# Optimization experiments

Measured on AMD Instinct MI355X. Metric: run time of the kernel, lower is better.

Reference implementation:

```python
import jax, jax.numpy as jnp
import numpy as np

HIDDEN = 384
NDIM = 3
N_POINTS = 100000
N_SUPER = 2048
MAX_DEG = 32
RADIUS = 0.045
INPUT_DIM = 3


def _sincos_embed(coords):
    # ContinuousSincosEmbed: dim=384, ndim=3 -> 128 channels per spatial dim (64 sin + 64 cos)
    eff = HIDDEN // NDIM  # 128
    omega = jnp.arange(0, eff, 2, dtype=jnp.float32) / eff
    freq = 1.0 / (10000.0 ** omega)  # [eff//2]
    out = coords[..., None] * freq  # [..., ndim, eff//2]
    emb = jnp.concatenate([jnp.sin(out), jnp.cos(out)], axis=-1)  # [..., ndim, eff]
    return emb.reshape(coords.shape[:-1] + (HIDDEN,))


def _radius_neighbors(pos, sn_idx):
    # numpy preprocessing equivalent of torch_geometric.nn.pool.radius with
    # max_num_neighbors=MAX_DEG; fixed-size padded [S, K] output + validity mask.
    nbr = np.zeros((N_SUPER, MAX_DEG), np.int32)
    mask = np.zeros((N_SUPER, MAX_DEG), bool)
    pos2 = (pos ** 2).sum(-1)
    r2 = RADIUS * RADIUS
    chunk = 128
    for i0 in range(0, N_SUPER, chunk):
        sp = pos[sn_idx[i0:i0 + chunk]]
        d2 = (sp ** 2).sum(-1)[:, None] + pos2[None, :] - 2.0 * (sp @ pos.T)
        within = d2 <= r2
        for j in range(sp.shape[0]):
            idx = np.nonzero(within[j])[0][:MAX_DEG]
            nbr[i0 + j, :len(idx)] = idx
            mask[i0 + j, :len(idx)] = True
    return nbr, mask


def setup_inputs() -> dict:
    rng = np.random.default_rng(0)
    pos = rng.random((N_POINTS, NDIM)).astype(np.float32)
    sn_idx = np.sort(rng.choice(N_POINTS, N_SUPER, replace=False)).astype(np.int32)
    nbr, mask = _radius_neighbors(pos, sn_idx)
    key = jax.random.key(0)
    ks = jax.random.split(key, 6)
    s = 0.02  # truncnormal002 init scale
    return {
        "input_pos": jnp.asarray(pos),
        "input_feat": jax.random.normal(ks[0], (N_POINTS, INPUT_DIM), jnp.float32),
        "supernode_idx": jnp.asarray(sn_idx),
        "neighbor_idx": jnp.asarray(nbr),
        "neighbor_mask": jnp.asarray(mask),
        "W_in": jax.random.normal(ks[1], (INPUT_DIM, HIDDEN), jnp.float32) * s,
        "b_in": jnp.zeros((HIDDEN,), jnp.float32),
        "W1": jax.random.normal(ks[2], (2 * HIDDEN, HIDDEN), jnp.float32) * s,
        "b1": jnp.zeros((HIDDEN,), jnp.float32),
        "W2": jax.random.normal(ks[3], (HIDDEN, HIDDEN), jnp.float32) * s,
        "b2": jnp.zeros((HIDDEN,), jnp.float32),
        "W_proj": jax.random.normal(ks[4], (2 * HIDDEN, HIDDEN), jnp.float32) * s,
        "b_proj": jnp.zeros((HIDDEN,), jnp.float32),
    }


def reference(input_pos, input_feat, supernode_idx, neighbor_idx, neighbor_mask,
              W_in, b_in, W1, b1, W2, b2, W_proj, b_proj):
    # point embeddings: continuous sincos pos embed + input feature projection
    x = _sincos_embed(input_pos) + input_feat @ W_in + b_in          # [N, D]
    sn = x[supernode_idx]                                            # [S, D] supernode pos embed
    src = x[neighbor_idx]                                            # [S, K, D] gathered neighbors
    dst = jnp.broadcast_to(sn[:, None, :], src.shape)                # [S, K, D]
    h = jnp.concatenate([src, dst], axis=-1)                         # [S, K, 2D]
    # message MLP (Linear -> GELU(exact) -> Linear), as nn.GELU default
    h = jax.nn.gelu(h @ W1 + b1, approximate=False) @ W2 + b2        # [S, K, D]
    # masked mean == segment_csr(..., reduce='mean') over variable-degree edges
    m = neighbor_mask[..., None].astype(h.dtype)
    agg = (h * m).sum(axis=1) / jnp.maximum(m.sum(axis=1), 1.0)      # [S, D]
    # readd_supernode_pos: concat supernode pos embed, project 2D -> D
    out = jnp.concatenate([agg, sn], axis=-1) @ W_proj + b_proj      # [S, D]
    return out[None]                                                 # [1, S, D] (batch_size=1)
```

## Files before the change

### kernel.cpp

```cpp
#include <hip/hip_runtime.h>
#include <hip/hip_bf16.h>
#include <cstdint>

#define HIDDEN 384
#define NSUPER 2048
#define MAXDEG 32
#define FRAGS (12*24*64)
#define WBLK  (FRAGS*8)

typedef __attribute__((ext_vector_type(8))) short bf16x8;
typedef __attribute__((ext_vector_type(4))) float f32x4;

__device__ inline unsigned short f2bf(float f) {
    __hip_bfloat16 h = __float2bfloat16(f);
    return *reinterpret_cast<unsigned short*>(&h);
}
__device__ inline float b2f(unsigned short s) {
    return __uint_as_float(((unsigned int)s) << 16);
}
__device__ inline bf16x8 pack8(const float* v) {
    union { bf16x8 v8; unsigned short u[8]; } u;
    #pragma unroll
    for (int i = 0; i < 8; ++i) u.u[i] = f2bf(v[i]);
    return u.v8;
}
__device__ inline float fast_erf(float x) {
    float ax = fabsf(x);
    float t  = 1.0f / fmaf(0.3275911f, ax, 1.0f);
    float p  = t*(0.254829592f + t*(-0.284496736f + t*(1.421413741f +
               t*(-1.453152027f + t*1.061405429f))));
    float e  = __expf(-ax*ax);
    return copysignf(1.0f - p*e, x);
}
__device__ inline float gelu(float y) {
    return 0.5f * y * (1.0f + fast_erf(y * 0.70710678118654752f));
}

__global__ __launch_bounds__(256)
void prep(const float* __restrict__ W1, const float* __restrict__ W2,
          const float* __restrict__ Wp, const unsigned int* __restrict__ mask,
          const float* __restrict__ pos, const float* __restrict__ feat,
          const int* __restrict__ sn_idx,
          const float* __restrict__ W_in, const float* __restrict__ b_in,
          unsigned short* __restrict__ w1sf, unsigned short* __restrict__ w1df,
          unsigned short* __restrict__ w2f,  unsigned short* __restrict__ wpf,
          unsigned short* __restrict__ snxb, int* __restrict__ flag) {
    const int b = blockIdx.x;
    const int t = threadIdx.x;
    if (b == 360) {
        __shared__ int s;
        if (t == 0) s = 0;
        __syncthreads();
        int bad = 0;
        for (int i = t; i < 16384; i += 256)
            if (mask[i] > 1u) bad = 1;
        if (bad) s = 1;
        __syncthreads();
        if (t == 0) *flag = s;
        return;
    }
    if (b > 360) {
        __shared__ float W4[HIDDEN][4];
        __shared__ float P6[64][7];
        const int eb = b - 361;
        if (t < 64) {
            const int pi = sn_idx[eb*64 + t];
            P6[t][0]=pos[pi*3];  P6[t][1]=pos[pi*3+1];  P6[t][2]=pos[pi*3+2];
            P6[t][3]=feat[pi*3]; P6[t][4]=feat[pi*3+1]; P6[t][5]=feat[pi*3+2];
        }
        for (int d = t; d < HIDDEN; d += 256) {
            W4[d][0]=W_in[d]; W4[d][1]=W_in[HIDDEN+d];
            W4[d][2]=W_in[2*HIDDEN+d]; W4[d][3]=b_in[d];
        }
        __syncthreads();
        const int er = t >> 2, seg = t & 3;
        float frA[8], frB[8];
        #pragma unroll
        for (int i = 0; i < 8; ++i) {
            frA[i] = exp2f(-(float)(seg*8 + i)      * 0.2076205059304601f);
            frB[i] = exp2f(-(float)(32 + seg*8 + i) * 0.2076205059304601f);
        }
        const float f0 = P6[er][3], f1 = P6[er][4], f2 = P6[er][5];
        #pragma unroll
        for (int cc = 0; cc < 3; ++cc) {
            const float pc = P6[er][cc];
            float sL[8], sH[8], cL[8], cH[8];
            #pragma unroll
            for (int i = 0; i < 8; ++i) {
                const float aL = pc*frA[i], aH = pc*frB[i];
                sL[i]=__sinf(aL); sH[i]=__sinf(aH); cL[i]=__cosf(aL); cH[i]=__cosf(aH);
            }
            #pragma unroll
            for (int q = 0; q < 4; ++q) {
                const float* bb = (q==0)?sL:(q==1)?sH:(q==2)?cL:cH;
                const int blk = cc*4 + q;
                float v[8];
                #pragma unroll
                for (int i = 0; i < 8; ++i) {
                    const int dim = blk*32 + seg*8 + i;
                    const float4 wv = *(const float4*)W4[dim];
                    v[i] = fmaf(f0, wv.x, fmaf(f1, wv.y, fmaf(f2, wv.z, bb[i] + wv.w)));
                }
                *(bf16x8*)&snxb[(size_t)(eb*64 + er)*HIDDEN + blk*32 + seg*8] = pack8(v);
            }
        }
        return;
    }
    const int grp = b / 72, sub = b % 72;
    const float* W; unsigned short* out;
    switch (grp) {
        case 0: W = W1;              out = w1sf; break;
        case 1: W = W1 + 384*HIDDEN; out = w1df; break;
        case 2: W = W2;              out = w2f;  break;
        case 3: W = Wp;              out = wpf;  break;
        default:W = Wp + 384*HIDDEN; out = wpf + WBLK; break;
    }
    const int idx = sub * 256 + t;
    const int l   = idx & 63;
    const int frag= idx >> 6;
    const int nt  = frag % 24;
    const int kt  = frag / 24;
    const int col = nt * 16 + (l & 15);
    const int k0  = kt * 32 + (l >> 4) * 8;
    unsigned int pk[4];
    #pragma unroll
    for (int j = 0; j < 4; ++j) {
        unsigned int lo = f2bf(W[(k0 + 2*j)     * HIDDEN + col]);
        unsigned int hi = f2bf(W[(k0 + 2*j + 1) * HIDDEN + col]);
        pk[j] = lo | (hi << 16);
    }
    *reinterpret_cast<uint4*>(&out[(size_t)idx * 8]) =
        *reinterpret_cast<const uint4*>(pk);
}

__global__ __launch_bounds__(256)
void k_dstv(const unsigned short* __restrict__ snxb,
            const unsigned short* __restrict__ w1df,
            const float* __restrict__ b1, float* __restrict__ dstv) {
    const int rg = blockIdx.x >> 2, cq = blockIdx.x & 3;
    const int t = threadIdx.x, w = t>>6, l = t&63, lg = l>>4, l15 = l&15;
    const int wgm = w>>1, wgn = w&1;
    const int r0 = rg*64 + wgm*32;
    const int ntb = cq*6 + wgn*3;
    f32x4 acc[2][3];
    #pragma unroll
    for (int mt=0; mt<2; ++mt)
        #pragma unroll
        for (int nt=0; nt<3; ++nt) acc[mt][nt] = (f32x4){0.f,0.f,0.f,0.f};
    #pragma unroll 2
    for (int kt = 0; kt < 12; ++kt) {
        bf16x8 a[2], bfr[3];
        const unsigned short* bpp = &w1df[((size_t)(kt*24 + ntb)*64 + l)*8];
        #pragma unroll
        for (int nt=0; nt<3; ++nt) bfr[nt] = *(const bf16x8*)(bpp + (size_t)nt*512);
        #pragma unroll
        for (int mt=0; mt<2; ++mt)
            a[mt] = *(const bf16x8*)&snxb[(size_t)(r0 + mt*16 + l15)*HIDDEN + kt*32 + lg*8];
        #pragma unroll
        for (int mt=0; mt<2; ++mt)
            #pragma unroll
            for (int nt=0; nt<3; ++nt)
                acc[mt][nt] = __builtin_amdgcn_mfma_f32_16x16x32_bf16(a[mt], bfr[nt], acc[mt][nt], 0,0,0);
    }
    #pragma unroll
    for (int mt=0; mt<2; ++mt)
        #pragma unroll
        for (int nt=0; nt<3; ++nt) {
            const int col = cq*96 + wgn*48 + nt*16 + l15;
            #pragma unroll
            for (int r=0; r<4; ++r) {
                const int row = r0 + mt*16 + lg*4 + r;
                dstv[(size_t)row*HIDDEN + col] = acc[mt][nt][r] + b1[col];
            }
        }
}

__global__ __launch_bounds__(256, 2)
void k_mlp(const float* __restrict__ pos, const float* __restrict__ feat,
           const int* __restrict__ nbr_idx, const void* __restrict__ mask_raw,
           const int* __restrict__ mask_fmt,
           const float* __restrict__ W_in, const float* __restrict__ b_in,
           const float* __restrict__ dstv,
           const unsigned short* __restrict__ W1f,
           const unsigned short* __restrict__ W2f,
           const float* __restrict__ b2, unsigned short* __restrict__ aggb)
{
    __shared__ unsigned short G[4*12*64*8];
    __shared__ ushort4 WINTB[HIDDEN];
    __shared__ float PF[64][7];
    __shared__ float CNT[2];

    const int t  = threadIdx.x;
    const int bm = blockIdx.x;
    const int l = t & 63, ng = t >> 6, lg = l >> 4, l15 = l & 15;

    float dvreg[2][6];
    #pragma unroll
    for (int sl = 0; sl < 2; ++sl)
        #pragma unroll
        for (int nt = 0; nt < 6; ++nt)
            dvreg[sl][nt] = dstv[(size_t)(bm*2 + sl)*HIDDEN + ng*96 + nt*16 + l15];

    bf16x8 bA[6], bB[6];
    #define LOADB(dst, Wf, kt)                                                  \
        { const unsigned short* bp_ = &Wf[((size_t)((kt)*24 + ng*6)*64 + l)*8]; \
          _Pragma("unroll")                                                     \
          for (int nt_ = 0; nt_ < 6; ++nt_)                                     \
              dst[nt_] = *(const bf16x8*)(bp_ + (size_t)nt_*512); }
    #define AREAD(a_, kt)                                                       \
        { _Pragma("unroll")                                                     \
          for (int mt_ = 0; mt_ < 4; ++mt_)                                     \
              a_[mt_] = *(const bf16x8*)&G[(size_t)(((mt_*12 + (kt))*64) + l)*8]; }
    #define MFMA6(bfr, a_)                                                      \
        { __builtin_amdgcn_s_setprio(1);                                        \
          _Pragma("unroll")                                                     \
          for (int mt_ = 0; mt_ < 4; ++mt_)                                     \
              _Pragma("unroll")                                                 \
              for (int nt_ = 0; nt_ < 6; ++nt_)                                 \
                  acc[mt_][nt_] = __builtin_amdgcn_mfma_f32_16x16x32_bf16(      \
                      a_[mt_], bfr[nt_], acc[mt_][nt_], 0, 0, 0);               \
          __builtin_amdgcn_s_setprio(0); }

    LOADB(bA, W1f, 0);

    if (t < 64) {
        const int e  = bm*64 + t;
        const int pi = nbr_idx[e];
        PF[t][0]=pos[pi*3];  PF[t][1]=pos[pi*3+1];  PF[t][2]=pos[pi*3+2];
        PF[t][3]=feat[pi*3]; PF[t][4]=feat[pi*3+1]; PF[t][5]=feat[pi*3+2];
        const int fmt = *mask_fmt;
        const int mv  = fmt ? (int)((const unsigned char*)mask_raw)[e]
                            : ((const int*)mask_raw)[e];
        PF[t][6] = mv ? 1.0f : 0.0f;
    }
    for (int d = t; d < HIDDEN; d += 256) {
        ushort4 wv;
        wv.x = f2bf(W_in[d]); wv.y = f2bf(W_in[HIDDEN+d]);
        wv.z = f2bf(W_in[2*HIDDEN+d]); wv.w = f2bf(b_in[d]);
        WINTB[d] = wv;
    }
    __syncthreads();
    if (t < 2) {
        float c = 0.f;
        for (int s = 0; s < 32; ++s) c += PF[t*32+s][6];
        CNT[t] = c;
    }

    const int er = t >> 2, seg = t & 3;
    float frA[8], frB[8];
    #pragma unroll
    for (int i = 0; i < 8; ++i) {
        frA[i] = exp2f(-(float)(seg*8 + i)      * 0.2076205059304601f);
        frB[i] = exp2f(-(float)(32 + seg*8 + i) * 0.2076205059304601f);
    }
    const float f0 = PF[er][3], f1 = PF[er][4], f2 = PF[er][5];
    const float pc0 = PF[er][0], pc1 = PF[er][1], pc2 = PF[er][2];
    const int slotbase = (er>>4)*12*64 + seg*16 + (er&15);

    #define EMB(kt_)                                                            \
        { const float pc = ((kt_)>>2)==0 ? pc0 : (((kt_)>>2)==1 ? pc1 : pc2);   \
          float v[8];                                                           \
          _Pragma("unroll")                                                     \
          for (int i = 0; i < 8; ++i) {                                         \
              const float fr = ((kt_)&1) ? frB[i] : frA[i];                     \
              const float aa = pc * fr;                                         \
              const float base = (((kt_)>>1)&1) ? __cosf(aa) : __sinf(aa);      \
              const ushort4 wv = WINTB[(kt_)*32 + seg*8 + i];                   \
              v[i] = fmaf(f0, b2f(wv.x), fmaf(f1, b2f(wv.y),                    \
                     fmaf(f2, b2f(wv.z), base + b2f(wv.w))));                   \
          }                                                                     \
          *(bf16x8*)&G[(size_t)(slotbase + (kt_)*64)*8] = pack8(v); }

    EMB(0);
    __syncthreads();

    f32x4 acc[4][6];
    #pragma unroll
    for (int mt=0; mt<4; ++mt)
        #pragma unroll
        for (int nt=0; nt<6; ++nt) acc[mt][nt] = (f32x4){0.f,0.f,0.f,0.f};

    #pragma unroll
    for (int kt = 0; kt < 12; kt += 2) {
        bf16x8 a[4];
        AREAD(a, kt);
        LOADB(bB, W1f, kt + 1);
        EMB(kt + 1);
        MFMA6(bA, a);
        __syncthreads();
        AREAD(a, kt + 1);
        if (kt + 2 < 12) { LOADB(bA, W1f, kt + 2); EMB(kt + 2); }
        MFMA6(bB, a);
        __syncthreads();
    }

    #pragma unroll
    for (int mt=0; mt<4; ++mt) {
        const int sl = mt >> 1;
        #pragma unroll
        for (int nt=0; nt<6; ++nt) {
            const int col = ng*96 + nt*16 + l15;
            const float dv = dvreg[sl][nt];
            const int base = ((mt*12 + (col>>5))*64 + ((col>>3)&3)*16 + lg*4)*8 + (col&7);
            #pragma unroll
            for (int r=0; r<4; ++r)
                G[base + r*8] = f2bf(gelu(acc[mt][nt][r] + dv));
        }
    }
    __syncthreads();

    #pragma unroll
    for (int mt=0; mt<4; ++mt)
        #pragma unroll
        for (int nt=0; nt<6; ++nt) acc[mt][nt] = (f32x4){0.f,0.f,0.f,0.f};
    LOADB(bA, W2f, 0); LOADB(bB, W2f, 1);
    #pragma unroll
    for (int kt = 0; kt < 12; kt += 2) {
        bf16x8 a[4];
        AREAD(a, kt);
        MFMA6(bA, a);
        if (kt + 2 < 12) LOADB(bA, W2f, kt + 2);
        AREAD(a, kt + 1);
        MFMA6(bB, a);
        if (kt + 3 < 12) LOADB(bB, W2f, kt + 3);
    }

    #pragma unroll
    for (int nt=0; nt<6; ++nt) {
        const int col = ng*96 + nt*16 + l15;
        float s0 = 0.f, s1 = 0.f;
        #pragma unroll
        for (int mt=0; mt<4; ++mt) {
            float p = 0.f;
            #pragma unroll
            for (int r=0; r<4; ++r)
                p += PF[mt*16 + lg*4 + r][6] * acc[mt][nt][r];
            if (mt < 2) s0 += p; else s1 += p;
        }
        s0 += __shfl_xor(s0,16); s0 += __shfl_xor(s0,32);
        s1 += __shfl_xor(s1,16); s1 += __shfl_xor(s1,32);
        if (lg == 0) {
            const float bb = b2[col];
            const int sn0 = bm*2;
            const float c0 = CNT[0], c1 = CNT[1];
            aggb[(size_t)sn0*HIDDEN + col]     = f2bf(s0 / fmaxf(c0,1.f) + bb*(c0>0.f?1.f:0.f));
            aggb[(size_t)(sn0+1)*HIDDEN + col] = f2bf(s1 / fmaxf(c1,1.f) + bb*(c1>0.f?1.f:0.f));
        }
    }
    #undef LOADB
    #undef AREAD
    #undef MFMA6
    #undef EMB
}

__global__ __launch_bounds__(256)
void k_proj(const unsigned short* __restrict__ aggb,
            const unsigned short* __restrict__ snxb,
            const unsigned short* __restrict__ wpf,
            const float* __restrict__ bp, float* __restrict__ out) {
    const int rg = blockIdx.x >> 2, cq = blockIdx.x & 3;
    const int t = threadIdx.x, w = t>>6, l = t&63, lg = l>>4, l15 = l&15;
    const int wgm = w>>1, wgn = w&1;
    const int r0 = rg*64 + wgm*32;
    const int ntb = cq*6 + wgn*3;
    f32x4 acc[2][3];
    #pragma unroll
    for (int mt=0; mt<2; ++mt)
        #pragma unroll
        for (int nt=0; nt<3; ++nt) acc[mt][nt] = (f32x4){0.f,0.f,0.f,0.f};
    #pragma unroll 2
    for (int kt = 0; kt < 24; ++kt) {
        const unsigned short* Ab = (kt < 12) ? aggb : snxb;
        const unsigned short* Wb = (kt < 12) ? wpf  : wpf + WBLK;
        const int ktt = (kt < 12) ? kt : kt - 12;
        bf16x8 a[2], bfr[3];
        const unsigned short* bpp = &Wb[((size_t)(ktt*24 + ntb)*64 + l)*8];
        #pragma unroll
        for (int nt=0; nt<3; ++nt) bfr[nt] = *(const bf16x8*)(bpp + (size_t)nt*512);
        #pragma unroll
        for (int mt=0; mt<2; ++mt)
            a[mt] = *(const bf16x8*)&Ab[(size_t)(r0 + mt*16 + l15)*HIDDEN + ktt*32 + lg*8];
        #pragma unroll
        for (int mt=0; mt<2; ++mt)
            #pragma unroll
            for (int nt=0; nt<3; ++nt)
                acc[mt][nt] = __builtin_amdgcn_mfma_f32_16x16x32_bf16(a[mt], bfr[nt], acc[mt][nt], 0,0,0);
    }
    #pragma unroll
    for (int mt=0; mt<2; ++mt)
        #pragma unroll
        for (int nt=0; nt<3; ++nt) {
            const int col = cq*96 + wgn*48 + nt*16 + l15;
            #pragma unroll
            for (int r=0; r<4; ++r) {
                const int row = r0 + mt*16 + lg*4 + r;
                out[(size_t)row*HIDDEN + col] = acc[mt][nt][r] + bp[col];
            }
        }
}

extern "C" void kernel_launch(void* const* d_in, const int* in_sizes, int n_in,
                              void* d_out, int out_size, void* d_ws, size_t ws_size,
                              hipStream_t stream) {
    const float* pos   = (const float*)d_in[0];
    const float* feat  = (const float*)d_in[1];
    const int*   sn    = (const int*)d_in[2];
    const int*   nbr   = (const int*)d_in[3];
    const void*  mask  = d_in[4];
    const float* W_in  = (const float*)d_in[5];
    const float* b_in  = (const float*)d_in[6];
    const float* W1    = (const float*)d_in[7];
    const float* b1    = (const float*)d_in[8];
    const float* W2    = (const float*)d_in[9];
    const float* b2    = (const float*)d_in[10];
    const float* Wp    = (const float*)d_in[11];
    const float* bpv   = (const float*)d_in[12];
    float* out = (float*)d_out;

    char* base = (char*)d_ws;
    int* flag = (int*)base;
    unsigned short* w1sf = (unsigned short*)(base + 256);
    unsigned short* w1df = w1sf + WBLK;
    unsigned short* w2f  = w1df + WBLK;
    unsigned short* wpf  = w2f  + WBLK;
    unsigned short* snxb = wpf  + 2*(size_t)WBLK;
    unsigned short* aggb = snxb + (size_t)NSUPER*HIDDEN;
    float* dstv = (float*)(aggb + (size_t)NSUPER*HIDDEN);

    hipLaunchKernelGGL(prep, dim3(393), dim3(256), 0, stream,
                       W1, W2, Wp, (const unsigned int*)mask,
                       pos, feat, sn, W_in, b_in,
                       w1sf, w1df, w2f, wpf, snxb, flag);
    hipLaunchKernelGGL(k_dstv, dim3(128), dim3(256), 0, stream,
                       snxb, w1df, b1, dstv);
    hipLaunchKernelGGL(k_mlp, dim3(1024), dim3(256), 0, stream,
                       pos, feat, nbr, mask, flag, W_in, b_in, dstv, w1sf, w2f, b2, aggb);
    hipLaunchKernelGGL(k_proj, dim3(128), dim3(256), 0, stream,
                       aggb, snxb, wpf, bpv, out);
}
```

Before: 90.24 us.

## Fuse supernode dst projection into message MLP kernel and use sigmoid-form GELU

Result: faster. 84.44 us (-6.4%).

```diff
diff --git a/kernel.cpp b/kernel.cpp
--- a/kernel.cpp
+++ b/kernel.cpp
@@ -12,8 +12,8 @@
 typedef __attribute__((ext_vector_type(4))) float f32x4;
 
 __device__ inline unsigned short f2bf(float f) {
-    __hip_bfloat16 h = __float2bfloat16(f);
-    return *reinterpret_cast<unsigned short*>(&h);
+    unsigned int u = __float_as_uint(f);
+    return (unsigned short)((u + 0x7fffu + ((u >> 16) & 1u)) >> 16);
 }
 __device__ inline float b2f(unsigned short s) {
     return __uint_as_float(((unsigned int)s) << 16);
@@ -24,16 +24,10 @@
     for (int i = 0; i < 8; ++i) u.u[i] = f2bf(v[i]);
     return u.v8;
 }
-__device__ inline float fast_erf(float x) {
-    float ax = fabsf(x);
-    float t  = 1.0f / fmaf(0.3275911f, ax, 1.0f);
-    float p  = t*(0.254829592f + t*(-0.284496736f + t*(1.421413741f +
-               t*(-1.453152027f + t*1.061405429f))));
-    float e  = __expf(-ax*ax);
-    return copysignf(1.0f - p*e, x);
-}
 __device__ inline float gelu(float y) {
-    return 0.5f * y * (1.0f + fast_erf(y * 0.70710678118654752f));
+    const float y2 = y * y;
+    const float m  = __expf(y * fmaf(-0.0713548163f, y2, -1.5957691216f));
+    return y * (1.0f / (1.0f + m));
 }
 
 __global__ __launch_bounds__(256)
@@ -133,57 +127,17 @@
         *reinterpret_cast<const uint4*>(pk);
 }
 
-__global__ __launch_bounds__(256)
-void k_dstv(const unsigned short* __restrict__ snxb,
-            const unsigned short* __restrict__ w1df,
-            const float* __restrict__ b1, float* __restrict__ dstv) {
-    const int rg = blockIdx.x >> 2, cq = blockIdx.x & 3;
-    const int t = threadIdx.x, w = t>>6, l = t&63, lg = l>>4, l15 = l&15;
-    const int wgm = w>>1, wgn = w&1;
-    const int r0 = rg*64 + wgm*32;
-    const int ntb = cq*6 + wgn*3;
-    f32x4 acc[2][3];
-    #pragma unroll
-    for (int mt=0; mt<2; ++mt)
-        #pragma unroll
-        for (int nt=0; nt<3; ++nt) acc[mt][nt] = (f32x4){0.f,0.f,0.f,0.f};
-    #pragma unroll 2
-    for (int kt = 0; kt < 12; ++kt) {
-        bf16x8 a[2], bfr[3];
-        const unsigned short* bpp = &w1df[((size_t)(kt*24 + ntb)*64 + l)*8];
-        #pragma unroll
-        for (int nt=0; nt<3; ++nt) bfr[nt] = *(const bf16x8*)(bpp + (size_t)nt*512);
-        #pragma unroll
-        for (int mt=0; mt<2; ++mt)
-            a[mt] = *(const bf16x8*)&snxb[(size_t)(r0 + mt*16 + l15)*HIDDEN + kt*32 + lg*8];
-        #pragma unroll
-        for (int mt=0; mt<2; ++mt)
-            #pragma unroll
-            for (int nt=0; nt<3; ++nt)
-                acc[mt][nt] = __builtin_amdgcn_mfma_f32_16x16x32_bf16(a[mt], bfr[nt], acc[mt][nt], 0,0,0);
-    }
-    #pragma unroll
-    for (int mt=0; mt<2; ++mt)
-        #pragma unroll
-        for (int nt=0; nt<3; ++nt) {
-            const int col = cq*96 + wgn*48 + nt*16 + l15;
-            #pragma unroll
-            for (int r=0; r<4; ++r) {
-                const int row = r0 + mt*16 + lg*4 + r;
-                dstv[(size_t)row*HIDDEN + col] = acc[mt][nt][r] + b1[col];
-            }
-        }
-}
-
 __global__ __launch_bounds__(256, 2)
 void k_mlp(const float* __restrict__ pos, const float* __restrict__ feat,
            const int* __restrict__ nbr_idx, const void* __restrict__ mask_raw,
            const int* __restrict__ mask_fmt,
            const float* __restrict__ W_in, const float* __restrict__ b_in,
-           const float* __restrict__ dstv,
-           const unsigned short* __restrict__ W1f,
+           const unsigned short* __restrict__ snxb,
+           const unsigned short* __restrict__ W1sf,
+           const unsigned short* __restrict__ W1df,
            const unsigned short* __restrict__ W2f,
-           const float* __restrict__ b2, unsigned short* __restrict__ aggb)
+           const float* __restrict__ b1, const float* __restrict__ b2,
+           unsigned short* __restrict__ aggb)
 {
     __shared__ unsigned short G[4*12*64*8];
     __shared__ ushort4 WINTB[HIDDEN];
@@ -193,13 +147,6 @@
     const int t  = threadIdx.x;
     const int bm = blockIdx.x;
     const int l = t & 63, ng = t >> 6, lg = l >> 4, l15 = l & 15;
-
-    float dvreg[2][6];
-    #pragma unroll
-    for (int sl = 0; sl < 2; ++sl)
-        #pragma unroll
-        for (int nt = 0; nt < 6; ++nt)
-            dvreg[sl][nt] = dstv[(size_t)(bm*2 + sl)*HIDDEN + ng*96 + nt*16 + l15];
 
     bf16x8 bA[6], bB[6];
     #define LOADB(dst, Wf, kt)                                                  \
@@ -221,8 +168,6 @@
                       a_[mt_], bfr[nt_], acc[mt_][nt_], 0, 0, 0);               \
           __builtin_amdgcn_s_setprio(0); }
 
-    LOADB(bA, W1f, 0);
-
     if (t < 64) {
         const int e  = bm*64 + t;
         const int pi = nbr_idx[e];
@@ -239,6 +184,9 @@
         wv.z = f2bf(W_in[2*HIDDEN+d]); wv.w = f2bf(b_in[d]);
         WINTB[d] = wv;
     }
+    float b1r[6];
+    #pragma unroll
+    for (int nt = 0; nt < 6; ++nt) b1r[nt] = b1[ng*96 + nt*16 + l15];
     __syncthreads();
     if (t < 2) {
         float c = 0.f;
@@ -271,40 +219,55 @@
           }                                                                     \
           *(bf16x8*)&G[(size_t)(slotbase + (kt_)*64)*8] = pack8(v); }
 
-    EMB(0);
+    f32x4 acc[4][6];
+    #pragma unroll
+    for (int mt=0; mt<4; ++mt)
+        #pragma unroll
+        for (int nt=0; nt<6; ++nt) acc[mt][nt] = (f32x4){0.f,0.f,0.f,0.f};
+
+    const unsigned short* snx0 = &snxb[(size_t)(bm*2 + 0)*HIDDEN];
+    const unsigned short* snx1 = &snxb[(size_t)(bm*2 + 1)*HIDDEN];
+    #pragma unroll
+    for (int kt = 0; kt < 12; ++kt) {
+        LOADB(bA, W1df, kt);
+        bf16x8 s0 = *(const bf16x8*)&snx0[kt*32 + lg*8];
+        bf16x8 s1 = *(const bf16x8*)&snx1[kt*32 + lg*8];
+        EMB(kt);
+        __builtin_amdgcn_s_setprio(1);
+        #pragma unroll
+        for (int nt = 0; nt < 6; ++nt) {
+            acc[0][nt] = __builtin_amdgcn_mfma_f32_16x16x32_bf16(s0, bA[nt], acc[0][nt], 0,0,0);
+            acc[1][nt] = __builtin_amdgcn_mfma_f32_16x16x32_bf16(s0, bA[nt], acc[1][nt], 0,0,0);
+            acc[2][nt] = __builtin_amdgcn_mfma_f32_16x16x32_bf16(s1, bA[nt], acc[2][nt], 0,0,0);
+            acc[3][nt] = __builtin_amdgcn_mfma_f32_16x16x32_bf16(s1, bA[nt], acc[3][nt], 0,0,0);
+        }
+        __builtin_amdgcn_s_setprio(0);
+    }
     __syncthreads();
 
-    f32x4 acc[4][6];
-    #pragma unroll
-    for (int mt=0; mt<4; ++mt)
-        #pragma unroll
-        for (int nt=0; nt<6; ++nt) acc[mt][nt] = (f32x4){0.f,0.f,0.f,0.f};
-
+    LOADB(bA, W1sf, 0); LOADB(bB, W1sf, 1);
     #pragma unroll
     for (int kt = 0; kt < 12; kt += 2) {
         bf16x8 a[4];
         AREAD(a, kt);
-        LOADB(bB, W1f, kt + 1);
-        EMB(kt + 1);
         MFMA6(bA, a);
-        __syncthreads();
+        if (kt + 2 < 12) LOADB(bA, W1sf, kt + 2);
         AREAD(a, kt + 1);
-        if (kt + 2 < 12) { LOADB(bA, W1f, kt + 2); EMB(kt + 2); }
         MFMA6(bB, a);
-        __syncthreads();
-    }
+        if (kt + 3 < 12) LOADB(bB, W1sf, kt + 3);
+    }
+    __syncthreads();
 
     #pragma unroll
     for (int mt=0; mt<4; ++mt) {
-        const int sl = mt >> 1;
         #pragma unroll
         for (int nt=0; nt<6; ++nt) {
             const int col = ng*96 + nt*16 + l15;
-            const float dv = dvreg[sl][nt];
+            const float bb1 = b1r[nt];
             const int base = ((mt*12 + (col>>5))*64 + ((col>>3)&3)*16 + lg*4)*8 + (col&7);
             #pragma unroll
             for (int r=0; r<4; ++r)
-                G[base + r*8] = f2bf(gelu(acc[mt][nt][r] + dv));
+                G[base + r*8] = f2bf(gelu(acc[mt][nt][r] + bb1));
         }
     }
     __syncthreads();
@@ -425,16 +388,14 @@
     unsigned short* wpf  = w2f  + WBLK;
     unsigned short* snxb = wpf  + 2*(size_t)WBLK;
     unsigned short* aggb = snxb + (size_t)NSUPER*HIDDEN;
-    float* dstv = (float*)(aggb + (size_t)NSUPER*HIDDEN);
 
     hipLaunchKernelGGL(prep, dim3(393), dim3(256), 0, stream,
                        W1, W2, Wp, (const unsigned int*)mask,
                        pos, feat, sn, W_in, b_in,
                        w1sf, w1df, w2f, wpf, snxb, flag);
-    hipLaunchKernelGGL(k_dstv, dim3(128), dim3(256), 0, stream,
-                       snxb, w1df, b1, dstv);
     hipLaunchKernelGGL(k_mlp, dim3(1024), dim3(256), 0, stream,
-                       pos, feat, nbr, mask, flag, W_in, b_in, dstv, w1sf, w2f, b2, aggb);
+                       pos, feat, nbr, mask, flag, W_in, b_in,
+                       snxb, w1sf, w1df, w2f, b1, b2, aggb);
     hipLaunchKernelGGL(k_proj, dim3(128), dim3(256), 0, stream,
                        aggb, snxb, wpf, bpv, out);
 }
```
